# Optimization experiments

Hardware: AMD Instinct MI355X
Metric: run time of the kernel (lower is better)

The kernel has to match this reference:

```python
import jax, jax.numpy as jnp
import numpy as np

DIM = 128
NUM_LAYERS = 5
EPS = 1e-5


def setup_inputs() -> dict:
    key = jax.random.key(0)
    ks = jax.random.split(key, 16)
    N, E, D = 50000, 640000, DIM
    x = jax.random.uniform(ks[0], (N, 3), dtype=jnp.float32)
    edge_index = jax.random.randint(ks[1], (2, E), 0, N, dtype=jnp.int64)
    norm = jax.random.uniform(ks[2], (E,), dtype=jnp.float32)
    s3 = 1.0 / np.sqrt(3.0)
    sd = 1.0 / np.sqrt(D)
    return {
        "x": x,
        "edge_index": edge_index,
        "norm": norm,
        "W_enc": jax.random.uniform(ks[3], (D, 3), jnp.float32, -s3, s3),
        "bn_e_gamma": jnp.ones((D,), jnp.float32),
        "bn_e_beta": jnp.zeros((D,), jnp.float32),
        "W_ih": jax.random.uniform(ks[4], (3 * D, D), jnp.float32, -sd, sd),
        "W_hh": jax.random.uniform(ks[5], (3 * D, D), jnp.float32, -sd, sd),
        "b_ih": jax.random.uniform(ks[6], (3 * D,), jnp.float32, -sd, sd),
        "b_hh": jax.random.uniform(ks[7], (3 * D,), jnp.float32, -sd, sd),
        "W_dec": jax.random.uniform(ks[8], (D // 2, D), jnp.float32, -sd, sd),
        "bn_d_gamma": jnp.ones((D // 2,), jnp.float32),
        "bn_d_beta": jnp.zeros((D // 2,), jnp.float32),
        "W_dec2": jax.random.uniform(ks[9], (1, D // 2), jnp.float32, -sd * np.sqrt(2.0), sd * np.sqrt(2.0)),
    }


def batchnorm(h, gamma, beta):
    # training-mode BatchNorm1d: biased batch stats over the node dimension
    mu = jnp.mean(h, axis=0)
    var = jnp.var(h, axis=0)
    return (h - mu) * jax.lax.rsqrt(var + EPS) * gamma + beta


def gru_cell(inp, hid, W_ih, W_hh, b_ih, b_hh):
    gi = inp @ W_ih.T + b_ih  # [N, 3D]
    gh = hid @ W_hh.T + b_hh
    D = hid.shape[1]
    i_r, i_z, i_n = gi[:, :D], gi[:, D:2 * D], gi[:, 2 * D:]
    h_r, h_z, h_n = gh[:, :D], gh[:, D:2 * D], gh[:, 2 * D:]
    r = jax.nn.sigmoid(i_r + h_r)
    z = jax.nn.sigmoid(i_z + h_z)
    n = jnp.tanh(i_n + r * h_n)
    return (1.0 - z) * n + z * hid


def reference(x, edge_index, norm, W_enc, bn_e_gamma, bn_e_beta, W_ih, W_hh, b_ih, b_hh, W_dec, bn_d_gamma, bn_d_beta, W_dec2):
    N = x.shape[0]
    src, dst = edge_index[0], edge_index[1]
    # encode
    h = jax.nn.relu(batchnorm(x @ W_enc.T, bn_e_gamma, bn_e_beta))  # [N, D]
    h_sum = h
    prev_h = h
    for _ in range(NUM_LAYERS):
        # neighborhood aggregation: scatter-add of norm-weighted source features
        msg = norm[:, None] * prev_h[src]  # [E, D]
        h_agg = jax.ops.segment_sum(msg, dst, num_segments=N)  # [N, D]
        h_sum = h_sum + h_agg
        prev_h = gru_cell(h_agg, prev_h, W_ih, W_hh, b_ih, b_hh)
    z = h_sum / (NUM_LAYERS + 1)  # mean over stacked h_list
    # decode
    y = jax.nn.relu(batchnorm(z @ W_dec.T, bn_d_gamma, bn_d_beta))
    y = y @ W_dec2.T  # [N, 1]
    return y.reshape(-1)
```

## Files before the change

### kernel.cpp

```cpp
#include <hip/hip_runtime.h>

#define DD 128

typedef _Float16 f16x8 __attribute__((ext_vector_type(8)));
typedef unsigned short u16x8 __attribute__((ext_vector_type(8)));
typedef unsigned short u16x4 __attribute__((ext_vector_type(4)));
typedef float f32x4 __attribute__((ext_vector_type(4)));

__device__ __forceinline__ float sigmoidf_(float v){ return 1.f/(1.f+__expf(-v)); }
__device__ __forceinline__ float tanhf_(float v){
  float e2 = __expf(2.f*v);
  return 1.f - 2.f/(e2 + 1.f);
}
__device__ __forceinline__ float h2f(unsigned short u){
  _Float16 h; __builtin_memcpy(&h, &u, 2); return (float)h;
}
__device__ __forceinline__ unsigned short f2h(float v){
  _Float16 h = (_Float16)v; unsigned short u; __builtin_memcpy(&u, &h, 2); return u;
}

__device__ __forceinline__ void gather_drain(const unsigned short* __restrict__ phc,
        const int2* __restrict__ csr, int i, int e, int q, float* acc){
  for (; i + 8 <= e; i += 8){
    int2 ed[8]; u16x8 R[8];
    #pragma unroll
    for (int u = 0; u < 8; u++) ed[u] = csr[i+u];
    #pragma unroll
    for (int u = 0; u < 8; u++) R[u] = *(const u16x8*)(phc + (size_t)ed[u].x*DD + q*8);
    #pragma unroll
    for (int u = 0; u < 8; u++){
      union { int i; float f; } c; c.i = ed[u].y;
      #pragma unroll
      for (int t = 0; t < 8; t++)
        acc[t] = fmaf(c.f, h2f((unsigned short)R[u][t]), acc[t]);
    }
  }
  if (i + 4 <= e){
    int2 ed[4]; u16x8 R[4];
    #pragma unroll
    for (int u = 0; u < 4; u++) ed[u] = csr[i+u];
    #pragma unroll
    for (int u = 0; u < 4; u++) R[u] = *(const u16x8*)(phc + (size_t)ed[u].x*DD + q*8);
    #pragma unroll
    for (int u = 0; u < 4; u++){
      union { int i; float f; } c; c.i = ed[u].y;
      #pragma unroll
      for (int t = 0; t < 8; t++)
        acc[t] = fmaf(c.f, h2f((unsigned short)R[u][t]), acc[t]);
    }
    i += 4;
  }
  for (; i < e; i++){
    int2 ed = csr[i];
    union { int i; float f; } c; c.i = ed.y;
    u16x8 R = *(const u16x8*)(phc + (size_t)ed.x*DD + q*8);
    #pragma unroll
    for (int t = 0; t < 8; t++)
      acc[t] = fmaf(c.f, h2f((unsigned short)R[t]), acc[t]);
  }
}

#define PREP_B 416
__global__ void __launch_bounds__(256) k_pre1(
        const float* __restrict__ W_ih, const float* __restrict__ W_hh,
        const float* __restrict__ W_dec, const float* __restrict__ x,
        const float* __restrict__ W_enc, const int* __restrict__ dst,
        unsigned short* __restrict__ Wih_h, unsigned short* __restrict__ Whh_h,
        unsigned short* __restrict__ Wd_h, unsigned short* __restrict__ h0,
        float* __restrict__ stats, int* __restrict__ counts, int N, int E){
  const int tid = threadIdx.x;
  const int gb = blockIdx.x;
  const int TOT = 384*128;
  if (gb < PREP_B){
    int idx = gb*256 + tid;
    if (idx < 2*TOT){
      const float* W = (idx < TOT) ? W_ih : W_hh;
      unsigned short* D = (idx < TOT) ? Wih_h : Whh_h;
      int fi = (idx < TOT) ? idx : idx - TOT;
      int t = fi & 7;
      int l = (fi >> 3) & 63;
      int ks = (fi >> 9) & 3;
      int nt = fi >> 11;
      int fg = nt / 3, gate = nt % 3;
      int j = gate*128 + fg*16 + (l & 15);
      int k = ks*32 + ((l >> 4) & 3)*8 + t;
      D[fi] = f2h(W[j*128 + k]);
    } else if (idx < 2*TOT + 64*128){
      int fi2 = idx - 2*TOT;
      int t  = fi2 & 7;
      int l  = (fi2 >> 3) & 63;
      int ks = (fi2 >> 9) & 3;
      int jt = fi2 >> 11;
      int j = jt*16 + (l & 15);
      int k = ks*32 + ((l >> 4) & 3)*8 + t;
      Wd_h[fi2] = f2h(W_dec[j*128 + k]);
    }
  } else if (gb < PREP_B + 256){
    const int b = gb - PREP_B;
    const int f = tid & 127;
    const int sub = tid >> 7;
    const float w0 = W_enc[f*3], w1 = W_enc[f*3+1], w2 = W_enc[f*3+2];
    const int chunk = (N + 255) / 256;
    const int n0 = b * chunk;
    const int n1 = (n0 + chunk < N) ? (n0 + chunk) : N;
    float s = 0.f, q = 0.f;
    for (int n = n0 + sub; n < n1; n += 2){
      float x0 = x[n*3], x1 = x[n*3+1], x2 = x[n*3+2];
      float h = x0*w0 + x1*w1 + x2*w2;
      unsigned short hu = f2h(h);
      float hq = h2f(hu);
      h0[(size_t)n*DD + f] = hu;
      s += hq; q += hq*hq;
    }
    atomicAdd(&stats[f], s);
    atomicAdd(&stats[DD+f], q);
  } else {
    int e = (gb - PREP_B - 256)*256 + tid;
    if (e < E) atomicAdd(&counts[dst[e]], 1);
  }
}

__global__ void __launch_bounds__(256) k_scan_part(const int* __restrict__ counts,
                                                   int* __restrict__ partials, int N){
  int i = blockIdx.x*256 + threadIdx.x;
  int v = (i < N) ? counts[i] : 0;
  #pragma unroll
  for (int off = 32; off > 0; off >>= 1) v += __shfl_down(v, off, 64);
  __shared__ int red[4];
  if ((threadIdx.x & 63) == 0) red[threadIdx.x >> 6] = v;
  __syncthreads();
  if (threadIdx.x == 0) partials[blockIdx.x] = red[0]+red[1]+red[2]+red[3];
}

__global__ void __launch_bounds__(256) k_scan_mid(int* __restrict__ partials, int P,
                                                  int* __restrict__ offsets, int N){
  __shared__ int lds[4];
  __shared__ int carry_s;
  const int lane = threadIdx.x & 63, wid = threadIdx.x >> 6;
  if (threadIdx.x == 0) carry_s = 0;
  __syncthreads();
  for (int base = 0; base < P; base += 256){
    int i = base + threadIdx.x;
    int v = (i < P) ? partials[i] : 0;
    int orig = v;
    #pragma unroll
    for (int off = 1; off < 64; off <<= 1){
      int u = __shfl_up(v, off, 64);
      if (lane >= off) v += u;
    }
    if (lane == 63) lds[wid] = v;
    __syncthreads();
    if (threadIdx.x == 0){
      int s = carry_s;
      for (int k = 0; k < 4; k++){ int t = lds[k]; lds[k] = s; s += t; }
      carry_s = s;
    }
    __syncthreads();
    int excl = v - orig + lds[wid];
    if (i < P) partials[i] = excl;
    __syncthreads();
  }
  if (threadIdx.x == 0) offsets[N] = carry_s;
}

__global__ void __launch_bounds__(256) k_scan_expand(const int* __restrict__ counts,
        const int* __restrict__ partials, int* __restrict__ offsets,
        int* __restrict__ cursors, int N){
  int i = blockIdx.x*256 + threadIdx.x;
  int v = (i < N) ? counts[i] : 0;
  int orig = v;
  const int lane = threadIdx.x & 63, wid = threadIdx.x >> 6;
  #pragma unroll
  for (int off = 1; off < 64; off <<= 1){
    int u = __shfl_up(v, off, 64);
    if (lane >= off) v += u;
  }
  __shared__ int lds[4];
  if (lane == 63) lds[wid] = v;
  __syncthreads();
  int wbase = 0;
  for (int k = 0; k < wid; k++) wbase += lds[k];
  int excl = partials[blockIdx.x] + wbase + v - orig;
  if (i < N){ offsets[i] = excl; cursors[i] = excl; }
}

__global__ void __launch_bounds__(256) k_pre2(
        const unsigned short* __restrict__ h0, const float* __restrict__ gamma,
        const float* __restrict__ beta, const float* __restrict__ stats,
        unsigned short* __restrict__ ph, unsigned short* __restrict__ hbn,
        const int* __restrict__ src, const int* __restrict__ dst,
        const float* __restrict__ norm, int* __restrict__ cursors,
        int2* __restrict__ csr, int N, int E, int AB){
  const int tid = threadIdx.x;
  if ((int)blockIdx.x < AB){
    int idx = blockIdx.x*256 + tid;
    if (idx >= N*DD) return;
    int f = idx & (DD-1);
    float invN = 1.f / (float)N;
    float mu = stats[f] * invN;
    float var = stats[DD+f] * invN - mu*mu;
    float v = (h2f(h0[idx]) - mu) * rsqrtf(var + 1e-5f) * gamma[f] + beta[f];
    v = fmaxf(v, 0.f);
    unsigned short hv = f2h(v);
    ph[idx] = hv;
    hbn[idx] = hv;
  } else {
    int e = ((int)blockIdx.x - AB)*256 + tid;
    if (e >= E) return;
    int p = atomicAdd(&cursors[dst[e]], 1);
    union { float f; int i; } c; c.f = norm[e];
    csr[p] = make_int2(src[e], c.i);
  }
}

__global__ void __launch_bounds__(256, 4) k_layer(
        const unsigned short* __restrict__ phc,
        unsigned short* __restrict__ phn,
        unsigned short* __restrict__ agg_out,
        const int* __restrict__ offsets, const int2* __restrict__ csr,
        const unsigned short* __restrict__ Wih_h, const unsigned short* __restrict__ Whh_h,
        const float* __restrict__ b_ih, const float* __restrict__ b_hh, int N){
  __shared__ unsigned short s_a[32*DD];
  const int tid = threadIdx.x;
  const int n0 = blockIdx.x * 32;

  {
    const int m = tid >> 4;
    const int q = tid & 15;
    const int nA = n0 + m;
    const int nB = n0 + 16 + m;
    float aA[8], aB[8];
    #pragma unroll
    for (int t = 0; t < 8; t++){ aA[t] = 0.f; aB[t] = 0.f; }
    int iA = 0, eA = 0, iB = 0, eB = 0;
    if (nA < N){ iA = offsets[nA]; eA = offsets[nA+1]; }
    if (nB < N){ iB = offsets[nB]; eB = offsets[nB+1]; }

    while (iA + 4 <= eA && iB + 4 <= eB){
      int2 edA[4], edB[4];
      #pragma unroll
      for (int u = 0; u < 4; u++){ edA[u] = csr[iA+u]; edB[u] = csr[iB+u]; }
      u16x8 RA[4], RB[4];
      #pragma unroll
      for (int u = 0; u < 4; u++){
        RA[u] = *(const u16x8*)(phc + (size_t)edA[u].x*DD + q*8);
        RB[u] = *(const u16x8*)(phc + (size_t)edB[u].x*DD + q*8);
      }
      #pragma unroll
      for (int u = 0; u < 4; u++){
        union { int i; float f; } cA, cB; cA.i = edA[u].y; cB.i = edB[u].y;
        #pragma unroll
        for (int t = 0; t < 8; t++){
          aA[t] = fmaf(cA.f, h2f((unsigned short)RA[u][t]), aA[t]);
          aB[t] = fmaf(cB.f, h2f((unsigned short)RB[u][t]), aB[t]);
        }
      }
      iA += 4; iB += 4;
    }
    gather_drain(phc, csr, iA, eA, q, aA);
    gather_drain(phc, csr, iB, eB, q, aB);

    u16x8 vA, vB;
    #pragma unroll
    for (int t = 0; t < 8; t++){ vA[t] = f2h(aA[t]); vB[t] = f2h(aB[t]); }
    if (nA < N) *(u16x8*)(agg_out + (size_t)nA*DD + q*8) = vA;
    if (nB < N) *(u16x8*)(agg_out + (size_t)nB*DD + q*8) = vB;
    const int ccA = q ^ (m & 7);
    *(u16x8*)(s_a + m*DD + ccA*8) = vA;
    *(u16x8*)(s_a + (16+m)*DD + ccA*8) = vB;
  }
  __syncthreads();

  const int w = tid >> 6, l = tid & 63, ar = l & 15, aq = l >> 4;
  int r0 = n0 + ar;      if (r0 >= N) r0 = N-1;
  int r1 = n0 + 16 + ar; if (r1 >= N) r1 = N-1;
  const size_t p0 = (size_t)r0*DD + aq*8;
  const size_t p1 = (size_t)r1*DD + aq*8;
  const int sw = ar & 7;

  for (int g = 0; g < 2; g++){
    const int fg = w*2 + g;
    f32x4 acc_i[2][3], acc_h[2][3];
    #pragma unroll
    for (int ta = 0; ta < 2; ta++)
      #pragma unroll
      for (int t = 0; t < 3; t++){
        acc_i[ta][t] = (f32x4){0.f,0.f,0.f,0.f};
        acc_h[ta][t] = (f32x4){0.f,0.f,0.f,0.f};
      }

    #pragma unroll
    for (int ks = 0; ks < 4; ks++){
      const int c = (ks*4 + aq) ^ sw;
      f16x8 ih0 = *(const f16x8*)(s_a + ar*DD       + c*8);
      f16x8 ih1 = *(const f16x8*)(s_a + (16+ar)*DD  + c*8);
      f16x8 hh0 = *(const f16x8*)(phc + p0 + ks*32);
      f16x8 hh1 = *(const f16x8*)(phc + p1 + ks*32);
      #pragma unroll
      for (int t = 0; t < 3; t++){
        size_t bo = ((size_t)((fg*3 + t)*4 + ks)*64 + l)*8;
        f16x8 bih = *(const f16x8*)(Wih_h + bo);
        f16x8 bhh = *(const f16x8*)(Whh_h + bo);
        acc_i[0][t] = __builtin_amdgcn_mfma_f32_16x16x32_f16(ih0, bih, acc_i[0][t], 0, 0, 0);
        acc_i[1][t] = __builtin_amdgcn_mfma_f32_16x16x32_f16(ih1, bih, acc_i[1][t], 0, 0, 0);
        acc_h[0][t] = __builtin_amdgcn_mfma_f32_16x16x32_f16(hh0, bhh, acc_h[0][t], 0, 0, 0);
        acc_h[1][t] = __builtin_amdgcn_mfma_f32_16x16x32_f16(hh1, bhh, acc_h[1][t], 0, 0, 0);
      }
    }

    const int f = fg*16 + ar;
    const float bir = b_ih[f], biz = b_ih[128+f], bin_ = b_ih[256+f];
    const float bhr = b_hh[f], bhz = b_hh[128+f], bhn = b_hh[256+f];
    #pragma unroll
    for (int ta = 0; ta < 2; ta++){
      #pragma unroll
      for (int r = 0; r < 4; r++){
        int n = n0 + ta*16 + aq*4 + r;
        if (n < N){
          float sir = acc_i[ta][0][r] + bir, shr = acc_h[ta][0][r] + bhr;
          float siz = acc_i[ta][1][r] + biz, shz = acc_h[ta][1][r] + bhz;
          float sin_ = acc_i[ta][2][r] + bin_, shn = acc_h[ta][2][r] + bhn;
          float rr = sigmoidf_(sir + shr);
          float zz = sigmoidf_(siz + shz);
          float nn = tanhf_(sin_ + rr*shn);
          size_t o = (size_t)n*DD + f;
          float hp = h2f(phc[o]);
          float h = (1.f - zz)*nn + zz*hp;
          phn[o] = f2h(h);
        }
      }
    }
  }
}

__global__ void __launch_bounds__(256, 8) k_dec1(const unsigned short* __restrict__ hbn,
        const unsigned short* __restrict__ aggs, size_t NF,
        const unsigned short* __restrict__ ph5,
        const int* __restrict__ offsets, const int2* __restrict__ csr,
        const unsigned short* __restrict__ Wd_h, unsigned short* __restrict__ y1,
        float* __restrict__ stats_d, int N){
  __shared__ unsigned short zs[16*DD];
  __shared__ unsigned short stage[16*64];
  const int tid = threadIdx.x;
  const int n0 = blockIdx.x * 16;

  {
    const int m = tid >> 4;
    const int q = tid & 15;
    const int n = n0 + m;
    float acc[8];
    #pragma unroll
    for (int t = 0; t < 8; t++) acc[t] = 0.f;
    if (n < N){
      size_t o = (size_t)n*DD + q*8;
      u16x8 hb = *(const u16x8*)(hbn + o);
      #pragma unroll
      for (int t = 0; t < 8; t++) acc[t] = h2f(hb[t]);
      #pragma unroll
      for (int l = 0; l < 4; l++){
        u16x8 ag = *(const u16x8*)(aggs + l*NF + o);
        #pragma unroll
        for (int t = 0; t < 8; t++) acc[t] += h2f(ag[t]);
      }
      gather_drain(ph5, csr, offsets[n], offsets[n+1], q, acc);
    }
    u16x8 vh;
    #pragma unroll
    for (int t = 0; t < 8; t++) vh[t] = f2h(acc[t] * (1.f/6.f));
    const int cc = q ^ (m & 7);
    *(u16x8*)(zs + m*DD + cc*8) = vh;
  }
  __syncthreads();

  const int w = tid >> 6, l = tid & 63, ar = l & 15, aq = l >> 4;
  const int sw = ar & 7;
  f32x4 acc = (f32x4){0.f,0.f,0.f,0.f};
  #pragma unroll
  for (int ks = 0; ks < 4; ks++){
    const int c = (ks*4 + aq) ^ sw;
    f16x8 a = *(const f16x8*)(zs + ar*DD + c*8);
    f16x8 b = *(const f16x8*)(Wd_h + ((size_t)(w*4 + ks)*64 + l)*8);
    acc = __builtin_amdgcn_mfma_f32_16x16x32_f16(a, b, acc, 0, 0, 0);
  }
  float s = 0.f, q2 = 0.f;
  #pragma unroll
  for (int r = 0; r < 4; r++){
    int n = n0 + aq*4 + r;
    float v = acc[r];
    if (n < N){
      stage[(aq*4 + r)*64 + w*16 + ar] = f2h(v);
      s += v; q2 += v*v;
    }
  }
  s  += __shfl_xor(s, 16, 64);  s  += __shfl_xor(s, 32, 64);
  q2 += __shfl_xor(q2, 16, 64); q2 += __shfl_xor(q2, 32, 64);
  if (aq == 0){
    float* st = stats_d + (size_t)(blockIdx.x & 7)*128;
    atomicAdd(&st[w*16 + ar], s);
    atomicAdd(&st[64 + w*16 + ar], q2);
  }
  __syncthreads();
  {
    int idx = tid * 4;
    int n = n0 + (idx >> 6);
    if (n < N)
      *(u16x4*)(y1 + (size_t)n0*64 + idx) = *(const u16x4*)(stage + idx);
  }
}

__global__ void __launch_bounds__(256) k_dec2(const unsigned short* __restrict__ y1,
        const float* __restrict__ gamma, const float* __restrict__ beta,
        const float* __restrict__ W_dec2, const float* __restrict__ stats_d,
        float* __restrict__ out, int N){
  const int j = threadIdx.x & 63;
  const int g = threadIdx.x >> 6;
  const int n = blockIdx.x*4 + g;
  if (n >= N) return;
  float ssum = 0.f, qsum = 0.f;
  #pragma unroll
  for (int c = 0; c < 8; c++){
    ssum += stats_d[c*128 + j];
    qsum += stats_d[c*128 + 64 + j];
  }
  float invN = 1.f / (float)N;
  float mu = ssum * invN;
  float var = qsum * invN - mu*mu;
  float v = (h2f(y1[(size_t)n*64 + j]) - mu) * rsqrtf(var + 1e-5f) * gamma[j] + beta[j];
  v = fmaxf(v, 0.f) * W_dec2[j];
  for (int off = 32; off > 0; off >>= 1) v += __shfl_down(v, off, 64);
  if (j == 0) out[n] = v;
}

extern "C" void kernel_launch(void* const* d_in, const int* in_sizes, int n_in,
                              void* d_out, int out_size, void* d_ws, size_t ws_size,
                              hipStream_t stream) {
  const int N = in_sizes[0] / 3;
  const int E = in_sizes[1] / 2;
  const int P = (N + 255) / 256;
  const int HIST_B = (E + 255) / 256;
  const int AB = (N*DD + 255) / 256;

  const float* x     = (const float*)d_in[0];
  const int*   ei    = (const int*)d_in[1];
  const int*   src   = ei;
  const int*   dst   = ei + E;
  const float* norm  = (const float*)d_in[2];
  const float* W_enc = (const float*)d_in[3];
  const float* g_e   = (const float*)d_in[4];
  const float* b_e   = (const float*)d_in[5];
  const float* W_ih  = (const float*)d_in[6];
  const float* W_hh  = (const float*)d_in[7];
  const float* b_ih  = (const float*)d_in[8];
  const float* b_hh  = (const float*)d_in[9];
  const float* W_dec = (const float*)d_in[10];
  const float* g_d   = (const float*)d_in[11];
  const float* b_d   = (const float*)d_in[12];
  const float* W_dec2= (const float*)d_in[13];
  float* out = (float*)d_out;

  float* ws = (float*)d_ws;
  const size_t NF = (size_t)N * DD;
  float* scr    = ws;
  unsigned short* h0h = (unsigned short*)scr;
  unsigned short* y1h = (unsigned short*)scr;
  float* stats  = scr + NF;
  float* Wt_dec = stats + 1280;
  unsigned short* Wd_h  = (unsigned short*)Wt_dec;
  unsigned short* Wih_h = (unsigned short*)(Wt_dec + 64*128);
  unsigned short* Whh_h = Wih_h + 384*128;
  unsigned short* ph_A  = Whh_h + 384*128;
  unsigned short* ph_B  = ph_A + NF;
  unsigned short* hbn   = ph_B + NF;
  unsigned short* aggs  = hbn + NF;
  int*   counts  = (int*)(aggs + 4*NF);
  int*   offsets = counts + N;
  int*   cursors = offsets + N + 1;
  int*   partials= cursors + N;
  int2*  csr     = (int2*)(partials + P);

  hipMemsetAsync(stats, 0, 1280*sizeof(float), stream);
  hipMemsetAsync(counts, 0, (size_t)N*sizeof(int), stream);

  k_pre1<<<PREP_B + 256 + HIST_B, 256, 0, stream>>>(
      W_ih, W_hh, W_dec, x, W_enc, dst,
      Wih_h, Whh_h, Wd_h, h0h, stats, counts, N, E);
  k_scan_part<<<P, 256, 0, stream>>>(counts, partials, N);
  k_scan_mid<<<1, 256, 0, stream>>>(partials, P, offsets, N);
  k_scan_expand<<<P, 256, 0, stream>>>(counts, partials, offsets, cursors, N);
  k_pre2<<<AB + HIST_B, 256, 0, stream>>>(
      h0h, g_e, b_e, stats, ph_A, hbn,
      src, dst, norm, cursors, csr, N, E, AB);

  unsigned short* phh_c = ph_A;
  unsigned short* phh_n = ph_B;
  for (int l = 0; l < 4; l++){
    k_layer<<<(N + 31)/32, 256, 0, stream>>>(phh_c, phh_n, aggs + (size_t)l*NF,
                                             offsets, csr,
                                             Wih_h, Whh_h, b_ih, b_hh, N);
    unsigned short* t = phh_c; phh_c = phh_n; phh_n = t;
  }

  k_dec1<<<(N + 15)/16, 256, 0, stream>>>(hbn, aggs, NF, phh_c, offsets, csr,
                                          Wd_h, y1h, stats + 256, N);
  k_dec2<<<(N + 3)/4, 256, 0, stream>>>(y1h, g_d, b_d, W_dec2, stats + 256, out, N);
}
```

Before: 477.8 us.

## Split fused gather+GRU layer kernel into separate gather and GRU kernels

The fused per-layer kernel is split in two. A lightweight gather kernel (128 threads, 8 nodes per block) does the CSR aggregation into a global agg buffer, and a separate GRU MFMA kernel reads agg straight from global memory. The GRU kernel now stages its output through shared memory so the stores are coalesced, and the fifth-layer aggregation moves out of the decoder into its own gather launch. The aim is better occupancy and load balance for the memory-bound gather, at the cost of extra launches and a global round trip of the aggregated features.

```diff
diff --git a/kernel.cpp b/kernel.cpp
--- a/kernel.cpp
+++ b/kernel.cpp
@@ -17,47 +17,6 @@
 }
 __device__ __forceinline__ unsigned short f2h(float v){
   _Float16 h = (_Float16)v; unsigned short u; __builtin_memcpy(&u, &h, 2); return u;
-}
-
-__device__ __forceinline__ void gather_drain(const unsigned short* __restrict__ phc,
-        const int2* __restrict__ csr, int i, int e, int q, float* acc){
-  for (; i + 8 <= e; i += 8){
-    int2 ed[8]; u16x8 R[8];
-    #pragma unroll
-    for (int u = 0; u < 8; u++) ed[u] = csr[i+u];
-    #pragma unroll
-    for (int u = 0; u < 8; u++) R[u] = *(const u16x8*)(phc + (size_t)ed[u].x*DD + q*8);
-    #pragma unroll
-    for (int u = 0; u < 8; u++){
-      union { int i; float f; } c; c.i = ed[u].y;
-      #pragma unroll
-      for (int t = 0; t < 8; t++)
-        acc[t] = fmaf(c.f, h2f((unsigned short)R[u][t]), acc[t]);
-    }
-  }
-  if (i + 4 <= e){
-    int2 ed[4]; u16x8 R[4];
-    #pragma unroll
-    for (int u = 0; u < 4; u++) ed[u] = csr[i+u];
-    #pragma unroll
-    for (int u = 0; u < 4; u++) R[u] = *(const u16x8*)(phc + (size_t)ed[u].x*DD + q*8);
-    #pragma unroll
-    for (int u = 0; u < 4; u++){
-      union { int i; float f; } c; c.i = ed[u].y;
-      #pragma unroll
-      for (int t = 0; t < 8; t++)
-        acc[t] = fmaf(c.f, h2f((unsigned short)R[u][t]), acc[t]);
-    }
-    i += 4;
-  }
-  for (; i < e; i++){
-    int2 ed = csr[i];
-    union { int i; float f; } c; c.i = ed.y;
-    u16x8 R = *(const u16x8*)(phc + (size_t)ed.x*DD + q*8);
-    #pragma unroll
-    for (int t = 0; t < 8; t++)
-      acc[t] = fmaf(c.f, h2f((unsigned short)R[t]), acc[t]);
-  }
 }
 
 #define PREP_B 416
@@ -213,70 +172,62 @@
   }
 }
 
-__global__ void __launch_bounds__(256, 4) k_layer(
+__global__ void __launch_bounds__(128, 8) k_gather(
+        const unsigned short* __restrict__ phc,
+        unsigned short* __restrict__ agg_out,
+        const int* __restrict__ offsets, const int2* __restrict__ csr, int N){
+  const int tid = threadIdx.x;
+  const int m = tid >> 4;
+  const int q = tid & 15;
+  const int n = blockIdx.x * 8 + m;
+  if (n >= N) return;
+  float acc[8];
+  #pragma unroll
+  for (int t = 0; t < 8; t++) acc[t] = 0.f;
+  int i = offsets[n];
+  const int e = offsets[n+1];
+  for (; i + 4 <= e; i += 4){
+    int2 ed[4]; u16x8 R[4];
+    #pragma unroll
+    for (int u = 0; u < 4; u++) ed[u] = csr[i+u];
+    #pragma unroll
+    for (int u = 0; u < 4; u++) R[u] = *(const u16x8*)(phc + (size_t)ed[u].x*DD + q*8);
+    #pragma unroll
+    for (int u = 0; u < 4; u++){
+      union { int i; float f; } c; c.i = ed[u].y;
+      #pragma unroll
+      for (int t = 0; t < 8; t++)
+        acc[t] = fmaf(c.f, h2f((unsigned short)R[u][t]), acc[t]);
+    }
+  }
+  for (; i < e; i++){
+    int2 ed = csr[i];
+    union { int i; float f; } c; c.i = ed.y;
+    u16x8 R = *(const u16x8*)(phc + (size_t)ed.x*DD + q*8);
+    #pragma unroll
+    for (int t = 0; t < 8; t++)
+      acc[t] = fmaf(c.f, h2f((unsigned short)R[t]), acc[t]);
+  }
+  u16x8 vh;
+  #pragma unroll
+  for (int t = 0; t < 8; t++) vh[t] = f2h(acc[t]);
+  *(u16x8*)(agg_out + (size_t)n*DD + q*8) = vh;
+}
+
+__global__ void __launch_bounds__(256, 4) k_gru(
         const unsigned short* __restrict__ phc,
         unsigned short* __restrict__ phn,
-        unsigned short* __restrict__ agg_out,
-        const int* __restrict__ offsets, const int2* __restrict__ csr,
+        const unsigned short* __restrict__ agg,
         const unsigned short* __restrict__ Wih_h, const unsigned short* __restrict__ Whh_h,
         const float* __restrict__ b_ih, const float* __restrict__ b_hh, int N){
-  __shared__ unsigned short s_a[32*DD];
+  __shared__ unsigned short s_st[32*DD];
   const int tid = threadIdx.x;
   const int n0 = blockIdx.x * 32;
-
-  {
-    const int m = tid >> 4;
-    const int q = tid & 15;
-    const int nA = n0 + m;
-    const int nB = n0 + 16 + m;
-    float aA[8], aB[8];
-    #pragma unroll
-    for (int t = 0; t < 8; t++){ aA[t] = 0.f; aB[t] = 0.f; }
-    int iA = 0, eA = 0, iB = 0, eB = 0;
-    if (nA < N){ iA = offsets[nA]; eA = offsets[nA+1]; }
-    if (nB < N){ iB = offsets[nB]; eB = offsets[nB+1]; }
-
-    while (iA + 4 <= eA && iB + 4 <= eB){
-      int2 edA[4], edB[4];
-      #pragma unroll
-      for (int u = 0; u < 4; u++){ edA[u] = csr[iA+u]; edB[u] = csr[iB+u]; }
-      u16x8 RA[4], RB[4];
-      #pragma unroll
-      for (int u = 0; u < 4; u++){
-        RA[u] = *(const u16x8*)(phc + (size_t)edA[u].x*DD + q*8);
-        RB[u] = *(const u16x8*)(phc + (size_t)edB[u].x*DD + q*8);
-      }
-      #pragma unroll
-      for (int u = 0; u < 4; u++){
-        union { int i; float f; } cA, cB; cA.i = edA[u].y; cB.i = edB[u].y;
-        #pragma unroll
-        for (int t = 0; t < 8; t++){
-          aA[t] = fmaf(cA.f, h2f((unsigned short)RA[u][t]), aA[t]);
-          aB[t] = fmaf(cB.f, h2f((unsigned short)RB[u][t]), aB[t]);
-        }
-      }
-      iA += 4; iB += 4;
-    }
-    gather_drain(phc, csr, iA, eA, q, aA);
-    gather_drain(phc, csr, iB, eB, q, aB);
-
-    u16x8 vA, vB;
-    #pragma unroll
-    for (int t = 0; t < 8; t++){ vA[t] = f2h(aA[t]); vB[t] = f2h(aB[t]); }
-    if (nA < N) *(u16x8*)(agg_out + (size_t)nA*DD + q*8) = vA;
-    if (nB < N) *(u16x8*)(agg_out + (size_t)nB*DD + q*8) = vB;
-    const int ccA = q ^ (m & 7);
-    *(u16x8*)(s_a + m*DD + ccA*8) = vA;
-    *(u16x8*)(s_a + (16+m)*DD + ccA*8) = vB;
-  }
-  __syncthreads();
-
   const int w = tid >> 6, l = tid & 63, ar = l & 15, aq = l >> 4;
   int r0 = n0 + ar;      if (r0 >= N) r0 = N-1;
   int r1 = n0 + 16 + ar; if (r1 >= N) r1 = N-1;
   const size_t p0 = (size_t)r0*DD + aq*8;
   const size_t p1 = (size_t)r1*DD + aq*8;
-  const int sw = ar & 7;
 
   for (int g = 0; g < 2; g++){
     const int fg = w*2 + g;
@@ -291,9 +242,8 @@
 
     #pragma unroll
     for (int ks = 0; ks < 4; ks++){
-      const int c = (ks*4 + aq) ^ sw;
-      f16x8 ih0 = *(const f16x8*)(s_a + ar*DD       + c*8);
-      f16x8 ih1 = *(const f16x8*)(s_a + (16+ar)*DD  + c*8);
+      f16x8 ih0 = *(const f16x8*)(agg + p0 + ks*32);
+      f16x8 ih1 = *(const f16x8*)(agg + p1 + ks*32);
       f16x8 hh0 = *(const f16x8*)(phc + p0 + ks*32);
       f16x8 hh1 = *(const f16x8*)(phc + p1 + ks*32);
       #pragma unroll
@@ -323,20 +273,25 @@
           float rr = sigmoidf_(sir + shr);
           float zz = sigmoidf_(siz + shz);
           float nn = tanhf_(sin_ + rr*shn);
-          size_t o = (size_t)n*DD + f;
-          float hp = h2f(phc[o]);
-          float h = (1.f - zz)*nn + zz*hp;
-          phn[o] = f2h(h);
+          float hp = h2f(phc[(size_t)n*DD + f]);
+          s_st[(ta*16 + aq*4 + r)*DD + f] = f2h((1.f - zz)*nn + zz*hp);
         }
       }
     }
   }
-}
-
-__global__ void __launch_bounds__(256, 8) k_dec1(const unsigned short* __restrict__ hbn,
+  __syncthreads();
+  {
+    int base = tid * 16;
+    int row = base >> 7;
+    if (n0 + row < N){
+      *(u16x8*)(phn + (size_t)n0*DD + base)     = *(const u16x8*)(s_st + base);
+      *(u16x8*)(phn + (size_t)n0*DD + base + 8) = *(const u16x8*)(s_st + base + 8);
+    }
+  }
+}
+
+__global__ void __launch_bounds__(256, 8) k_dec(const unsigned short* __restrict__ hbn,
         const unsigned short* __restrict__ aggs, size_t NF,
-        const unsigned short* __restrict__ ph5,
-        const int* __restrict__ offsets, const int2* __restrict__ csr,
         const unsigned short* __restrict__ Wd_h, unsigned short* __restrict__ y1,
         float* __restrict__ stats_d, int N){
   __shared__ unsigned short zs[16*DD];
@@ -357,12 +312,11 @@
       #pragma unroll
       for (int t = 0; t < 8; t++) acc[t] = h2f(hb[t]);
       #pragma unroll
-      for (int l = 0; l < 4; l++){
+      for (int l = 0; l < 5; l++){
         u16x8 ag = *(const u16x8*)(aggs + l*NF + o);
         #pragma unroll
         for (int t = 0; t < 8; t++) acc[t] += h2f(ag[t]);
       }
-      gather_drain(ph5, csr, offsets[n], offsets[n+1], q, acc);
     }
     u16x8 vh;
     #pragma unroll
@@ -472,7 +426,7 @@
   unsigned short* ph_B  = ph_A + NF;
   unsigned short* hbn   = ph_B + NF;
   unsigned short* aggs  = hbn + NF;
-  int*   counts  = (int*)(aggs + 4*NF);
+  int*   counts  = (int*)(aggs + 5*NF);
   int*   offsets = counts + N;
   int*   cursors = offsets + N + 1;
   int*   partials= cursors + N;
@@ -493,14 +447,17 @@
 
   unsigned short* phh_c = ph_A;
   unsigned short* phh_n = ph_B;
+  const int GB = (N + 7) / 8;
+  const int UB = (N + 31) / 32;
   for (int l = 0; l < 4; l++){
-    k_layer<<<(N + 31)/32, 256, 0, stream>>>(phh_c, phh_n, aggs + (size_t)l*NF,
-                                             offsets, csr,
-                                             Wih_h, Whh_h, b_ih, b_hh, N);
+    unsigned short* agg_l = aggs + (size_t)l*NF;
+    k_gather<<<GB, 128, 0, stream>>>(phh_c, agg_l, offsets, csr, N);
+    k_gru<<<UB, 256, 0, stream>>>(phh_c, phh_n, agg_l,
+                                  Wih_h, Whh_h, b_ih, b_hh, N);
     unsigned short* t = phh_c; phh_c = phh_n; phh_n = t;
   }
-
-  k_dec1<<<(N + 15)/16, 256, 0, stream>>>(hbn, aggs, NF, phh_c, offsets, csr,
-                                          Wd_h, y1h, stats + 256, N);
+  k_gather<<<GB, 128, 0, stream>>>(phh_c, aggs + (size_t)4*NF, offsets, csr, N);
+
+  k_dec<<<(N + 15)/16, 256, 0, stream>>>(hbn, aggs, NF, Wd_h, y1h, stats + 256, N);
   k_dec2<<<(N + 3)/4, 256, 0, stream>>>(y1h, g_d, b_d, W_dec2, stats + 256, out, N);
 }
```

Result: slower. 501.6 us (+5.0%).
